# Kernel tuning notes

Measured on AMD Instinct MI355X. Metric: run time of the kernel, lower is better.

The kernel has to match this reference:

```python
import jax, jax.numpy as jnp
import numpy as np


def setup_inputs() -> dict:
    key = jax.random.key(0)
    k1, k2 = jax.random.split(key)
    q_embed = jax.random.normal(k1, (1000, 1024), dtype=jnp.float32)      # (V, D)
    conv_feat = jax.random.normal(k2, (64, 1024, 800), dtype=jnp.float32)  # (B, D, T)
    return {"q_embed": q_embed, "conv_feat": conv_feat}


def reference(q_embed, conv_feat):
    # sim_scores: (B, V, T) = q_embed (V, D) @ conv_feat (B, D, T), no scaling
    sim_scores = jnp.einsum('vd,bdt->bvt', q_embed, conv_feat)
    attention_weights = jax.nn.softmax(sim_scores, axis=2)  # over T
    # context: (B, V, D) = weights (B, V, T) @ conv_feat^T (B, T, D)
    context_vector = jnp.einsum('bvt,bdt->bvd', attention_weights, conv_feat)
    return (context_vector, attention_weights)
```

## Files before the change

kernel.cpp:

```cpp
#include <hip/hip_runtime.h>
#include <hip/hip_bf16.h>

typedef short bf16x8 __attribute__((ext_vector_type(8)));
typedef float f32x4 __attribute__((ext_vector_type(4)));

#define NV 1000
#define ND 1024
#define NT 800
#define NB 64

__device__ inline unsigned short f32_bf16(float f) {
    unsigned u = __builtin_bit_cast(unsigned, f);
    return (unsigned short)((u + 0x7FFFu + ((u >> 16) & 1u)) >> 16);
}
__device__ inline void split_bf16(float f, unsigned short& h, unsigned short& l) {
    unsigned u = __builtin_bit_cast(unsigned, f);
    unsigned hb = (u + 0x7FFFu + ((u >> 16) & 1u)) >> 16;
    h = (unsigned short)hb;
    float hf = __builtin_bit_cast(float, hb << 16);
    float lf = f - hf;
    unsigned ul = __builtin_bit_cast(unsigned, lf);
    l = (unsigned short)((ul + 0x7FFFu + ((ul >> 16) & 1u)) >> 16);
}

__device__ inline void gload16(const void* g, void* l) {
    __builtin_amdgcn_global_load_lds(
        (const __attribute__((address_space(1))) unsigned int*)g,
        (__attribute__((address_space(3))) unsigned int*)l, 16, 0, 0);
}

__global__ __launch_bounds__(256) void prep_q(const float* __restrict__ Q,
                                              unsigned short* __restrict__ Qh,
                                              unsigned short* __restrict__ Ql) {
    int idx = blockIdx.x * 256 + threadIdx.x;
    int row = idx >> 8;
    int c4 = (idx & 255) << 2;
    float4 f = make_float4(0.f, 0.f, 0.f, 0.f);
    if (row < NV) f = *(const float4*)(Q + (size_t)row * ND + c4);
    unsigned short h0,h1,h2,h3,l0,l1,l2,l3;
    split_bf16(f.x,h0,l0); split_bf16(f.y,h1,l1);
    split_bf16(f.z,h2,l2); split_bf16(f.w,h3,l3);
    *(ushort4*)(Qh + (size_t)row * ND + c4) = make_ushort4(h0,h1,h2,h3);
    *(ushort4*)(Ql + (size_t)row * ND + c4) = make_ushort4(l0,l1,l2,l3);
}

__global__ __launch_bounds__(256) void prep_c(const float* __restrict__ C,
                                              unsigned short* __restrict__ Cth,
                                              unsigned short* __restrict__ Ctl,
                                              unsigned short* __restrict__ Cbf,
                                              int writeCbf) {
    const int dt = blockIdx.x;
    const int tt = blockIdx.y;
    const int b  = blockIdx.z;
    const int tid = threadIdx.x;
    __shared__ float T[64][33];
    const float* Cb = C + (size_t)b * ND * NT;
    const int d0 = dt * 64, t0 = tt * 32;
#pragma unroll
    for (int r = 0; r < 2; ++r) {
        int idx = r * 256 + tid;
        int row = idx >> 3;
        int c4 = (idx & 7) << 2;
        float4 f = *(const float4*)(Cb + (size_t)(d0 + row) * NT + t0 + c4);
        T[row][c4 + 0] = f.x; T[row][c4 + 1] = f.y;
        T[row][c4 + 2] = f.z; T[row][c4 + 3] = f.w;
        if (writeCbf) {
            *(ushort4*)(Cbf + ((size_t)b * ND + d0 + row) * NT + t0 + c4) =
                make_ushort4(f32_bf16(f.x), f32_bf16(f.y), f32_bf16(f.z), f32_bf16(f.w));
        }
    }
    __syncthreads();
#pragma unroll
    for (int r = 0; r < 2; ++r) {
        int idx = r * 256 + tid;
        int trow = idx >> 4;
        int dc = (idx & 15) << 2;
        unsigned short h[4], l[4];
#pragma unroll
        for (int j = 0; j < 4; ++j) split_bf16(T[dc + j][trow], h[j], l[j]);
        size_t o = ((size_t)b * NT + t0 + trow) * ND + d0 + dc;
        *(ushort4*)(Cth + o) = make_ushort4(h[0],h[1],h[2],h[3]);
        *(ushort4*)(Ctl + o) = make_ushort4(l[0],l[1],l[2],l[3]);
    }
}

__global__ __launch_bounds__(512) void gemm1_kernel(const unsigned short* __restrict__ Qh,
                                                    const unsigned short* __restrict__ Ql,
                                                    const unsigned short* __restrict__ Cth,
                                                    const unsigned short* __restrict__ Ctl,
                                                    float* __restrict__ S) {
    const int h = blockIdx.x;
    const int L = (h & 7) * 160 + (h >> 3);
    const int bm = L & 3;
    const int rest = L >> 2;
    const int bn = rest % 5;
    const int b  = rest / 5;

    const int tid = threadIdx.x;
    const int lane = tid & 63;
    const int w = tid >> 6;
    const int wr = w >> 1, wc = w & 1;

    __shared__ unsigned short lds[2 * 26624];

    const int v0 = bm * 256, t0 = bn * 160;
    const unsigned short* Agh = Qh + (size_t)v0 * ND;
    const unsigned short* Agl = Ql + (size_t)v0 * ND;
    const unsigned short* Bgh = Cth + ((size_t)b * NT + t0) * ND;
    const unsigned short* Bgl = Ctl + ((size_t)b * NT + t0) * ND;

    f32x4 acc[4][5];
#pragma unroll
    for (int i = 0; i < 4; ++i)
#pragma unroll
        for (int j = 0; j < 5; ++j) acc[i][j] = (f32x4){0.f, 0.f, 0.f, 0.f};

    const int srow = lane >> 2;
    const int sslot = lane & 3;
    const int swz = (sslot ^ (srow & 3) ^ ((srow >> 2) & 3)) << 3;
    const int g = lane >> 4, rl = lane & 15;
    const int sx = (g ^ (rl & 3) ^ ((rl >> 2) & 3)) << 4;

    const unsigned short* srcB[7];
    int dstU[7];
#pragma unroll
    for (int j = 0; j < 7; ++j) {
        int R = w * 7 + j; if (R >= 52) R -= 52;
        const unsigned short* sp; int du;
        if (R < 16)      { sp = Agh + (size_t)(R * 16 + srow) * ND;          du = R * 512; }
        else if (R < 32) { sp = Agl + (size_t)((R - 16) * 16 + srow) * ND;   du = 8192 + (R - 16) * 512; }
        else if (R < 42) { sp = Bgh + (size_t)((R - 32) * 16 + srow) * ND;   du = 16384 + (R - 32) * 512; }
        else             { sp = Bgl + (size_t)((R - 42) * 16 + srow) * ND;   du = 21504 + (R - 42) * 512; }
        srcB[j] = sp + swz;
        dstU[j] = du;
    }

#define G1_STAGE(K0, BUF)                                                     \
    {                                                                         \
        unsigned short* Lb = lds + (BUF) * 26624;                             \
        _Pragma("unroll")                                                     \
        for (int j = 0; j < 7; ++j) gload16(srcB[j] + (K0), Lb + dstU[j]);    \
    }

#define G1_COMPUTE(BUF)                                                       \
    {                                                                         \
        const char* Lb = (const char*)(lds + (BUF) * 26624);                  \
        bf16x8 ah[4], al[4], bh[5], bl[5];                                    \
        _Pragma("unroll")                                                     \
        for (int mf = 0; mf < 4; ++mf) {                                      \
            int off = (wr * 64 + mf * 16 + rl) * 64 + sx;                     \
            ah[mf] = *(const bf16x8*)(Lb + off);                              \
            al[mf] = *(const bf16x8*)(Lb + 16384 + off);                      \
        }                                                                     \
        _Pragma("unroll")                                                     \
        for (int nf = 0; nf < 5; ++nf) {                                      \
            int off = (wc * 80 + nf * 16 + rl) * 64 + sx;                     \
            bh[nf] = *(const bf16x8*)(Lb + 32768 + off);                      \
            bl[nf] = *(const bf16x8*)(Lb + 43008 + off);                      \
        }                                                                     \
        _Pragma("unroll")                                                     \
        for (int mf = 0; mf < 4; ++mf)                                        \
            _Pragma("unroll")                                                 \
            for (int nf = 0; nf < 5; ++nf) {                                  \
                acc[mf][nf] = __builtin_amdgcn_mfma_f32_16x16x32_bf16(ah[mf], bh[nf], acc[mf][nf], 0, 0, 0); \
                acc[mf][nf] = __builtin_amdgcn_mfma_f32_16x16x32_bf16(ah[mf], bl[nf], acc[mf][nf], 0, 0, 0); \
                acc[mf][nf] = __builtin_amdgcn_mfma_f32_16x16x32_bf16(al[mf], bh[nf], acc[mf][nf], 0, 0, 0); \
            }                                                                 \
    }

    G1_STAGE(0, 0);
    int cur = 0;
#pragma unroll 1
    for (int t = 0; t < 31; ++t) {
        G1_STAGE((t + 1) * 32, cur ^ 1);
        asm volatile("s_waitcnt vmcnt(7)\n\ts_barrier" ::: "memory");
        G1_COMPUTE(cur);
        asm volatile("s_waitcnt lgkmcnt(0)\n\ts_barrier" ::: "memory");
        cur ^= 1;
    }
    asm volatile("s_waitcnt vmcnt(0)\n\ts_barrier" ::: "memory");
    G1_COMPUTE(cur);

    float* Sb = S + (size_t)b * NV * NT;
#pragma unroll
    for (int mf = 0; mf < 4; ++mf) {
#pragma unroll
        for (int nf = 0; nf < 5; ++nf) {
#pragma unroll
            for (int r = 0; r < 4; ++r) {
                int v = v0 + wr * 64 + mf * 16 + g * 4 + r;
                int t = t0 + wc * 80 + nf * 16 + rl;
                if (v < NV) Sb[(size_t)v * NT + t] = acc[mf][nf][r];
            }
        }
    }
#undef G1_STAGE
#undef G1_COMPUTE
}

__global__ __launch_bounds__(256) void softmax_kernel(float* __restrict__ S,
                                                      unsigned short* __restrict__ Wbf,
                                                      int writeWbf) {
    const int row = blockIdx.x * 4 + (threadIdx.x >> 6);
    const int lane = threadIdx.x & 63;
    float* p = S + (size_t)row * NT;
    unsigned short* pw = Wbf + (size_t)row * NT;
    float v[13];
    float m = -INFINITY;
#pragma unroll
    for (int i = 0; i < 13; ++i) {
        int t = i * 64 + lane;
        v[i] = (t < NT) ? p[t] : -INFINITY;
        m = fmaxf(m, v[i]);
    }
#pragma unroll
    for (int off = 32; off; off >>= 1) m = fmaxf(m, __shfl_xor(m, off));
    float s = 0.f;
#pragma unroll
    for (int i = 0; i < 13; ++i) {
        int t = i * 64 + lane;
        float e = (t < NT) ? __expf(v[i] - m) : 0.f;
        v[i] = e;
        s += e;
    }
#pragma unroll
    for (int off = 32; off; off >>= 1) s += __shfl_xor(s, off);
    const float inv = 1.0f / s;
#pragma unroll
    for (int i = 0; i < 13; ++i) {
        int t = i * 64 + lane;
        if (t < NT) {
            float wv = v[i] * inv;
            p[t] = wv;
            if (writeWbf) pw[t] = f32_bf16(wv);
        }
    }
}

__global__ __launch_bounds__(512) void gemm2_fast(const unsigned short* __restrict__ Wbf,
                                                  const unsigned short* __restrict__ Cbf,
                                                  float* __restrict__ O) {
    const int h = blockIdx.x;
    const int L = (h & 7) * 128 + (h >> 3);
    const int b  = L >> 4;
    const int bm = (L >> 2) & 3;
    const int bn = L & 3;
    const int tid = threadIdx.x;
    const int lane = tid & 63;
    const int w = tid >> 6;
    const int wr = w >> 2, wc = w & 3;

    __shared__ unsigned short lds[2 * 16384];

    const int v0 = bm * 256, d0 = bn * 256;
    const unsigned short* Ag = Wbf + (size_t)b * NV * NT;
    const unsigned short* Bg = Cbf + ((size_t)b * ND + d0) * NT;

    f32x4 acc[8][4];
#pragma unroll
    for (int i = 0; i < 8; ++i)
#pragma unroll
        for (int j = 0; j < 4; ++j) acc[i][j] = (f32x4){0.f, 0.f, 0.f, 0.f};

    const int srow = lane >> 2;
    const int sslot = lane & 3;
    const int swz = (sslot ^ (srow & 3) ^ ((srow >> 2) & 3)) << 3;
    const int g = lane >> 4, rl = lane & 15;
    const int sx = (g ^ (rl & 3) ^ ((rl >> 2) & 3)) << 4;

#define G2_STAGE(K0, BUF)                                                     \
    {                                                                         \
        unsigned short* Lb = lds + (BUF) * 16384;                             \
        _Pragma("unroll")                                                     \
        for (int i = w; i < 16; i += 8) {                                     \
            int row = i * 16 + srow;                                          \
            int vrow = v0 + row; if (vrow > NV - 1) vrow = NV - 1;            \
            gload16(Ag + (size_t)vrow * NT + swz + (K0), Lb + i * 512);       \
            gload16(Bg + (size_t)row * NT + swz + (K0), Lb + 8192 + i * 512); \
        }                                                                     \
    }

#define G2_COMPUTE(BUF)                                                       \
    {                                                                         \
        const char* Lb = (const char*)(lds + (BUF) * 16384);                  \
        bf16x8 a[8], bq[4];                                                   \
        _Pragma("unroll")                                                     \
        for (int mf = 0; mf < 8; ++mf) {                                      \
            int off = (wr * 128 + mf * 16 + rl) * 64 + sx;                    \
            a[mf] = *(const bf16x8*)(Lb + off);                               \
        }                                                                     \
        _Pragma("unroll")                                                     \
        for (int nf = 0; nf < 4; ++nf) {                                      \
            int off = (wc * 64 + nf * 16 + rl) * 64 + sx;                     \
            bq[nf] = *(const bf16x8*)(Lb + 16384 + off);                      \
        }                                                                     \
        _Pragma("unroll")                                                     \
        for (int mf = 0; mf < 8; ++mf)                                        \
            _Pragma("unroll")                                                 \
            for (int nf = 0; nf < 4; ++nf)                                    \
                acc[mf][nf] = __builtin_amdgcn_mfma_f32_16x16x32_bf16(a[mf], bq[nf], acc[mf][nf], 0, 0, 0); \
    }

    G2_STAGE(0, 0);
    int cur = 0;
#pragma unroll 1
    for (int t = 0; t < 24; ++t) {
        G2_STAGE((t + 1) * 32, cur ^ 1);
        asm volatile("s_waitcnt vmcnt(4)\n\ts_barrier" ::: "memory");
        G2_COMPUTE(cur);
        asm volatile("s_waitcnt lgkmcnt(0)\n\ts_barrier" ::: "memory");
        cur ^= 1;
    }
    asm volatile("s_waitcnt vmcnt(0)\n\ts_barrier" ::: "memory");
    G2_COMPUTE(cur);

    float* Ob = O + (size_t)b * NV * ND;
#pragma unroll
    for (int mf = 0; mf < 8; ++mf) {
#pragma unroll
        for (int nf = 0; nf < 4; ++nf) {
#pragma unroll
            for (int r = 0; r < 4; ++r) {
                int v = v0 + wr * 128 + mf * 16 + g * 4 + r;
                int d = d0 + wc * 64 + nf * 16 + rl;
                if (v < NV) Ob[(size_t)v * ND + d] = acc[mf][nf][r];
            }
        }
    }
#undef G2_STAGE
#undef G2_COMPUTE
}

__global__ __launch_bounds__(256) void gemm2_mid(const unsigned short* __restrict__ Wbf,
                                                 const float* __restrict__ C,
                                                 float* __restrict__ O) {
    const int h = blockIdx.x;
    const int L = (h & 7) * 512 + (h >> 3);
    const int bm = L & 7;
    const int bn = (L >> 3) & 7;
    const int b  = L >> 6;
    const int tid = threadIdx.x;
    const int lane = tid & 63;
    const int w = tid >> 6;
    const int wr = w >> 1, wc = w & 1;

    __shared__ unsigned short As[128 * 32];
    __shared__ unsigned short Bs[128][40];

    const int v0 = bm * 128, d0 = bn * 128;
    const unsigned short* Ag = Wbf + (size_t)b * NV * NT;
    const float* Cb = C + (size_t)b * ND * NT;

    f32x4 acc[4][4];
#pragma unroll
    for (int i = 0; i < 4; ++i)
#pragma unroll
        for (int j = 0; j < 4; ++j) acc[i][j] = (f32x4){0.f, 0.f, 0.f, 0.f};

    const int srow = lane >> 2;
    const int sslot = lane & 3;

    for (int k0 = 0; k0 < NT; k0 += 32) {
        for (int i = w; i < 8; i += 4) {
            int row = i * 16 + srow;
            int c = ((sslot ^ (row & 3)) << 3) + k0;
            int vrow = v0 + row; if (vrow > NV - 1) vrow = NV - 1;
            gload16(Ag + (size_t)vrow * NT + c, As + i * 512);
        }
#pragma unroll
        for (int r = 0; r < 4; ++r) {
            int idx = r * 256 + tid;
            int row = idx >> 3;
            int kq  = (idx & 7) << 2;
            const float4 f = *(const float4*)(Cb + (size_t)(d0 + row) * NT + k0 + kq);
            *(ushort4*)&Bs[row][kq] = make_ushort4(f32_bf16(f.x), f32_bf16(f.y), f32_bf16(f.z), f32_bf16(f.w));
        }
        __syncthreads();

        const int g = lane >> 4, rl = lane & 15;
        const int sx = (g ^ (rl & 3)) << 4;
        const int kk = g << 3;
        bf16x8 a[4], bfr[4];
#pragma unroll
        for (int mf = 0; mf < 4; ++mf) {
            int off = (wr * 64 + mf * 16 + rl) * 64 + sx;
            a[mf] = *(const bf16x8*)((const char*)As + off);
        }
#pragma unroll
        for (int nf = 0; nf < 4; ++nf) {
            int row = wc * 64 + nf * 16 + rl;
            bfr[nf] = *(const bf16x8*)&Bs[row][kk];
        }
#pragma unroll
        for (int mf = 0; mf < 4; ++mf)
#pragma unroll
            for (int nf = 0; nf < 4; ++nf)
                acc[mf][nf] = __builtin_amdgcn_mfma_f32_16x16x32_bf16(a[mf], bfr[nf], acc[mf][nf], 0, 0, 0);
        __syncthreads();
    }

    float* Ob = O + (size_t)b * NV * ND;
    const int g = lane >> 4, rl = lane & 15;
#pragma unroll
    for (int mf = 0; mf < 4; ++mf) {
#pragma unroll
        for (int nf = 0; nf < 4; ++nf) {
#pragma unroll
            for (int r = 0; r < 4; ++r) {
                int v = v0 + wr * 64 + mf * 16 + g * 4 + r;
                int d = d0 + wc * 64 + nf * 16 + rl;
                if (v < NV) Ob[(size_t)v * ND + d] = acc[mf][nf][r];
            }
        }
    }
}

__global__ __launch_bounds__(256) void gemm2_slow(const float* __restrict__ W,
                                                  const float* __restrict__ C,
                                                  float* __restrict__ O) {
    const int h = blockIdx.x;
    const int L = (h & 7) * 512 + (h >> 3);
    const int bm = L & 7;
    const int bn = (L >> 3) & 7;
    const int b  = L >> 6;
    const int tid = threadIdx.x;
    const int lane = tid & 63;
    const int wid = tid >> 6;
    const int wr = wid >> 1;
    const int wc = wid & 1;

    __shared__ unsigned short As[128][40];
    __shared__ unsigned short Bs[128][40];

    const float* Wb = W + (size_t)b * NV * NT;
    const float* Cb = C + (size_t)b * ND * NT;
    const int v0 = bm * 128;
    const int d0 = bn * 128;

    f32x4 acc[4][4];
#pragma unroll
    for (int i = 0; i < 4; ++i)
#pragma unroll
        for (int j = 0; j < 4; ++j) acc[i][j] = (f32x4){0.f, 0.f, 0.f, 0.f};

    for (int k0 = 0; k0 < NT; k0 += 32) {
#pragma unroll
        for (int r = 0; r < 4; ++r) {
            int idx = r * 256 + tid;
            int row = idx >> 3;
            int kq  = (idx & 7) << 2;
            int v = v0 + row; if (v > NV - 1) v = NV - 1;
            const float4 f = *(const float4*)(Wb + (size_t)v * NT + k0 + kq);
            *(ushort4*)&As[row][kq] = make_ushort4(f32_bf16(f.x), f32_bf16(f.y), f32_bf16(f.z), f32_bf16(f.w));
        }
#pragma unroll
        for (int r = 0; r < 4; ++r) {
            int idx = r * 256 + tid;
            int row = idx >> 3;
            int kq  = (idx & 7) << 2;
            const float4 f = *(const float4*)(Cb + (size_t)(d0 + row) * NT + k0 + kq);
            *(ushort4*)&Bs[row][kq] = make_ushort4(f32_bf16(f.x), f32_bf16(f.y), f32_bf16(f.z), f32_bf16(f.w));
        }
        __syncthreads();

        bf16x8 a[4], bfr[4];
        const int kk = (lane >> 4) << 3;
#pragma unroll
        for (int mf = 0; mf < 4; ++mf) {
            int row = wr * 64 + mf * 16 + (lane & 15);
            a[mf] = *(const bf16x8*)&As[row][kk];
        }
#pragma unroll
        for (int nf = 0; nf < 4; ++nf) {
            int row = wc * 64 + nf * 16 + (lane & 15);
            bfr[nf] = *(const bf16x8*)&Bs[row][kk];
        }
#pragma unroll
        for (int mf = 0; mf < 4; ++mf)
#pragma unroll
            for (int nf = 0; nf < 4; ++nf)
                acc[mf][nf] = __builtin_amdgcn_mfma_f32_16x16x32_bf16(a[mf], bfr[nf], acc[mf][nf], 0, 0, 0);
        __syncthreads();
    }

    float* Ob = O + (size_t)b * NV * ND;
#pragma unroll
    for (int mf = 0; mf < 4; ++mf) {
#pragma unroll
        for (int nf = 0; nf < 4; ++nf) {
#pragma unroll
            for (int r = 0; r < 4; ++r) {
                int v = v0 + wr * 64 + mf * 16 + (lane >> 4) * 4 + r;
                int d = d0 + wc * 64 + nf * 16 + (lane & 15);
                if (v < NV) Ob[(size_t)v * ND + d] = acc[mf][nf][r];
            }
        }
    }
}

extern "C" void kernel_launch(void* const* d_in, const int* in_sizes, int n_in,
                              void* d_out, int out_size, void* d_ws, size_t ws_size,
                              hipStream_t stream) {
    const float* Q = (const float*)d_in[0];
    const float* C = (const float*)d_in[1];
    float* ctx = (float*)d_out;
    float* wts = ctx + (size_t)NB * NV * ND;

    unsigned short* Cth = (unsigned short*)ctx;
    unsigned short* Ctl = Cth + (size_t)NB * NT * ND;
    unsigned short* Qh  = Ctl + (size_t)NB * NT * ND;
    unsigned short* Ql  = Qh + (size_t)1024 * ND;

    const size_t WbfBytes = (size_t)NB * NV * NT * 2;
    const size_t CbfBytes = (size_t)NB * ND * NT * 2;
    unsigned short* Wbf = (unsigned short*)d_ws;
    unsigned short* Cbf = (unsigned short*)((char*)d_ws + WbfBytes);
    const int wsFast = ws_size >= WbfBytes + CbfBytes;
    const int wsMid  = ws_size >= WbfBytes;

    prep_q<<<dim3(1024), 256, 0, stream>>>(Q, Qh, Ql);
    prep_c<<<dim3(16, 25, NB), 256, 0, stream>>>(C, Cth, Ctl, Cbf, wsFast);
    gemm1_kernel<<<dim3(1280), 512, 0, stream>>>(Qh, Ql, Cth, Ctl, wts);
    softmax_kernel<<<dim3(16000), 256, 0, stream>>>(wts, Wbf, wsMid);
    if (wsFast)      gemm2_fast<<<dim3(1024), 512, 0, stream>>>(Wbf, Cbf, ctx);
    else if (wsMid)  gemm2_mid<<<dim3(4096), 256, 0, stream>>>(Wbf, C, ctx);
    else             gemm2_slow<<<dim3(4096), 256, 0, stream>>>(wts, C, ctx);
}
```

Before: 658.1 us.

## Split GEMM inner loops into barrier-separated phases with MFMA priority; vectorize softmax

Both bf16 GEMM kernels now run their inner step as several phases. Each phase loads part of the LDS fragments, then issues MFMAs at raised s_setprio, with barriers and sched_barriers between phases. The goal is a ping-pong schedule in which one wave's LDS reads overlap with another wave's matrix math, and register pressure drops because fewer fragments are live at once. The cost is many more workgroup barriers per K step, which can serialize waves. Softmax is also switched to float4 loads and stores with packed bf16 writes, to cut memory instructions.

```diff
diff --git a/kernel.cpp b/kernel.cpp
--- a/kernel.cpp
+++ b/kernel.cpp
@@ -8,6 +8,9 @@
 #define ND 1024
 #define NT 800
 #define NB 64
+
+#define BARRIER asm volatile("s_barrier" ::: "memory")
+#define SB0 __builtin_amdgcn_sched_barrier(0)
 
 __device__ inline unsigned short f32_bf16(float f) {
     unsigned u = __builtin_bit_cast(unsigned, f);
@@ -135,6 +138,8 @@
         dstU[j] = du;
     }
 
+    bf16x8 ah[4], al[4], bh[5], bl[5];
+
 #define G1_STAGE(K0, BUF)                                                     \
     {                                                                         \
         unsigned short* Lb = lds + (BUF) * 26624;                             \
@@ -142,30 +147,45 @@
         for (int j = 0; j < 7; ++j) gload16(srcB[j] + (K0), Lb + dstU[j]);    \
     }
 
-#define G1_COMPUTE(BUF)                                                       \
+#define G1_PHASES(BUF)                                                        \
     {                                                                         \
         const char* Lb = (const char*)(lds + (BUF) * 26624);                  \
-        bf16x8 ah[4], al[4], bh[5], bl[5];                                    \
-        _Pragma("unroll")                                                     \
-        for (int mf = 0; mf < 4; ++mf) {                                      \
-            int off = (wr * 64 + mf * 16 + rl) * 64 + sx;                     \
-            ah[mf] = *(const bf16x8*)(Lb + off);                              \
-            al[mf] = *(const bf16x8*)(Lb + 16384 + off);                      \
-        }                                                                     \
-        _Pragma("unroll")                                                     \
-        for (int nf = 0; nf < 5; ++nf) {                                      \
-            int off = (wc * 80 + nf * 16 + rl) * 64 + sx;                     \
-            bh[nf] = *(const bf16x8*)(Lb + 32768 + off);                      \
-            bl[nf] = *(const bf16x8*)(Lb + 43008 + off);                      \
-        }                                                                     \
+        _Pragma("unroll")                                                     \
+        for (int mf = 0; mf < 4; ++mf)                                        \
+            ah[mf] = *(const bf16x8*)(Lb + (wr * 64 + mf * 16 + rl) * 64 + sx); \
+        _Pragma("unroll")                                                     \
+        for (int nf = 0; nf < 5; ++nf)                                        \
+            bh[nf] = *(const bf16x8*)(Lb + 32768 + (wc * 80 + nf * 16 + rl) * 64 + sx); \
+        BARRIER; SB0;                                                         \
+        __builtin_amdgcn_s_setprio(1);                                        \
         _Pragma("unroll")                                                     \
         for (int mf = 0; mf < 4; ++mf)                                        \
             _Pragma("unroll")                                                 \
-            for (int nf = 0; nf < 5; ++nf) {                                  \
+            for (int nf = 0; nf < 5; ++nf)                                    \
                 acc[mf][nf] = __builtin_amdgcn_mfma_f32_16x16x32_bf16(ah[mf], bh[nf], acc[mf][nf], 0, 0, 0); \
+        __builtin_amdgcn_s_setprio(0); SB0; BARRIER;                          \
+        _Pragma("unroll")                                                     \
+        for (int mf = 0; mf < 4; ++mf)                                        \
+            al[mf] = *(const bf16x8*)(Lb + 16384 + (wr * 64 + mf * 16 + rl) * 64 + sx); \
+        BARRIER; SB0;                                                         \
+        __builtin_amdgcn_s_setprio(1);                                        \
+        _Pragma("unroll")                                                     \
+        for (int mf = 0; mf < 4; ++mf)                                        \
+            _Pragma("unroll")                                                 \
+            for (int nf = 0; nf < 5; ++nf)                                    \
+                acc[mf][nf] = __builtin_amdgcn_mfma_f32_16x16x32_bf16(al[mf], bh[nf], acc[mf][nf], 0, 0, 0); \
+        __builtin_amdgcn_s_setprio(0); SB0; BARRIER;                          \
+        _Pragma("unroll")                                                     \
+        for (int nf = 0; nf < 5; ++nf)                                        \
+            bl[nf] = *(const bf16x8*)(Lb + 43008 + (wc * 80 + nf * 16 + rl) * 64 + sx); \
+        BARRIER; SB0;                                                         \
+        __builtin_amdgcn_s_setprio(1);                                        \
+        _Pragma("unroll")                                                     \
+        for (int mf = 0; mf < 4; ++mf)                                        \
+            _Pragma("unroll")                                                 \
+            for (int nf = 0; nf < 5; ++nf)                                    \
                 acc[mf][nf] = __builtin_amdgcn_mfma_f32_16x16x32_bf16(ah[mf], bl[nf], acc[mf][nf], 0, 0, 0); \
-                acc[mf][nf] = __builtin_amdgcn_mfma_f32_16x16x32_bf16(al[mf], bh[nf], acc[mf][nf], 0, 0, 0); \
-            }                                                                 \
+        __builtin_amdgcn_s_setprio(0); SB0; BARRIER;                          \
     }
 
     G1_STAGE(0, 0);
@@ -173,13 +193,14 @@
 #pragma unroll 1
     for (int t = 0; t < 31; ++t) {
         G1_STAGE((t + 1) * 32, cur ^ 1);
-        asm volatile("s_waitcnt vmcnt(7)\n\ts_barrier" ::: "memory");
-        G1_COMPUTE(cur);
-        asm volatile("s_waitcnt lgkmcnt(0)\n\ts_barrier" ::: "memory");
+        asm volatile("s_waitcnt vmcnt(7)" ::: "memory");
+        BARRIER;
+        G1_PHASES(cur);
         cur ^= 1;
     }
-    asm volatile("s_waitcnt vmcnt(0)\n\ts_barrier" ::: "memory");
-    G1_COMPUTE(cur);
+    asm volatile("s_waitcnt vmcnt(0)" ::: "memory");
+    BARRIER;
+    G1_PHASES(cur);
 
     float* Sb = S + (size_t)b * NV * NT;
 #pragma unroll
@@ -195,7 +216,7 @@
         }
     }
 #undef G1_STAGE
-#undef G1_COMPUTE
+#undef G1_PHASES
 }
 
 __global__ __launch_bounds__(256) void softmax_kernel(float* __restrict__ S,
@@ -203,36 +224,42 @@
                                                       int writeWbf) {
     const int row = blockIdx.x * 4 + (threadIdx.x >> 6);
     const int lane = threadIdx.x & 63;
-    float* p = S + (size_t)row * NT;
+    float4* p4 = (float4*)(S + (size_t)row * NT);
     unsigned short* pw = Wbf + (size_t)row * NT;
-    float v[13];
+    float4 v[4];
     float m = -INFINITY;
 #pragma unroll
-    for (int i = 0; i < 13; ++i) {
-        int t = i * 64 + lane;
-        v[i] = (t < NT) ? p[t] : -INFINITY;
-        m = fmaxf(m, v[i]);
+    for (int i = 0; i < 4; ++i) {
+        int idx = i * 64 + lane;
+        if (idx < 200) {
+            v[i] = p4[idx];
+            m = fmaxf(m, fmaxf(fmaxf(v[i].x, v[i].y), fmaxf(v[i].z, v[i].w)));
+        }
     }
 #pragma unroll
     for (int off = 32; off; off >>= 1) m = fmaxf(m, __shfl_xor(m, off));
     float s = 0.f;
 #pragma unroll
-    for (int i = 0; i < 13; ++i) {
-        int t = i * 64 + lane;
-        float e = (t < NT) ? __expf(v[i] - m) : 0.f;
-        v[i] = e;
-        s += e;
+    for (int i = 0; i < 4; ++i) {
+        int idx = i * 64 + lane;
+        if (idx < 200) {
+            v[i].x = __expf(v[i].x - m); v[i].y = __expf(v[i].y - m);
+            v[i].z = __expf(v[i].z - m); v[i].w = __expf(v[i].w - m);
+            s += (v[i].x + v[i].y) + (v[i].z + v[i].w);
+        }
     }
 #pragma unroll
     for (int off = 32; off; off >>= 1) s += __shfl_xor(s, off);
     const float inv = 1.0f / s;
 #pragma unroll
-    for (int i = 0; i < 13; ++i) {
-        int t = i * 64 + lane;
-        if (t < NT) {
-            float wv = v[i] * inv;
-            p[t] = wv;
-            if (writeWbf) pw[t] = f32_bf16(wv);
+    for (int i = 0; i < 4; ++i) {
+        int idx = i * 64 + lane;
+        if (idx < 200) {
+            float4 o = make_float4(v[i].x * inv, v[i].y * inv, v[i].z * inv, v[i].w * inv);
+            p4[idx] = o;
+            if (writeWbf)
+                *(ushort4*)(pw + idx * 4) =
+                    make_ushort4(f32_bf16(o.x), f32_bf16(o.y), f32_bf16(o.z), f32_bf16(o.w));
         }
     }
 }
@@ -268,6 +295,8 @@
     const int g = lane >> 4, rl = lane & 15;
     const int sx = (g ^ (rl & 3) ^ ((rl >> 2) & 3)) << 4;
 
+    bf16x8 a2[8], bq2[4];
+
 #define G2_STAGE(K0, BUF)                                                     \
     {                                                                         \
         unsigned short* Lb = lds + (BUF) * 16384;                             \
@@ -280,25 +309,34 @@
         }                                                                     \
     }
 
-#define G2_COMPUTE(BUF)                                                       \
+#define G2_PHASES(BUF)                                                        \
     {                                                                         \
         const char* Lb = (const char*)(lds + (BUF) * 16384);                  \
-        bf16x8 a[8], bq[4];                                                   \
-        _Pragma("unroll")                                                     \
-        for (int mf = 0; mf < 8; ++mf) {                                      \
-            int off = (wr * 128 + mf * 16 + rl) * 64 + sx;                    \
-            a[mf] = *(const bf16x8*)(Lb + off);                               \
-        }                                                                     \
-        _Pragma("unroll")                                                     \
-        for (int nf = 0; nf < 4; ++nf) {                                      \
-            int off = (wc * 64 + nf * 16 + rl) * 64 + sx;                     \
-            bq[nf] = *(const bf16x8*)(Lb + 16384 + off);                      \
-        }                                                                     \
-        _Pragma("unroll")                                                     \
-        for (int mf = 0; mf < 8; ++mf)                                        \
+        _Pragma("unroll")                                                     \
+        for (int mf = 0; mf < 4; ++mf)                                        \
+            a2[mf] = *(const bf16x8*)(Lb + (wr * 128 + mf * 16 + rl) * 64 + sx); \
+        _Pragma("unroll")                                                     \
+        for (int nf = 0; nf < 4; ++nf)                                        \
+            bq2[nf] = *(const bf16x8*)(Lb + 16384 + (wc * 64 + nf * 16 + rl) * 64 + sx); \
+        BARRIER; SB0;                                                         \
+        __builtin_amdgcn_s_setprio(1);                                        \
+        _Pragma("unroll")                                                     \
+        for (int mf = 0; mf < 4; ++mf)                                        \
             _Pragma("unroll")                                                 \
             for (int nf = 0; nf < 4; ++nf)                                    \
-                acc[mf][nf] = __builtin_amdgcn_mfma_f32_16x16x32_bf16(a[mf], bq[nf], acc[mf][nf], 0, 0, 0); \
+                acc[mf][nf] = __builtin_amdgcn_mfma_f32_16x16x32_bf16(a2[mf], bq2[nf], acc[mf][nf], 0, 0, 0); \
+        __builtin_amdgcn_s_setprio(0); SB0; BARRIER;                          \
+        _Pragma("unroll")                                                     \
+        for (int mf = 4; mf < 8; ++mf)                                        \
+            a2[mf] = *(const bf16x8*)(Lb + (wr * 128 + mf * 16 + rl) * 64 + sx); \
+        BARRIER; SB0;                                                         \
+        __builtin_amdgcn_s_setprio(1);                                        \
+        _Pragma("unroll")                                                     \
+        for (int mf = 4; mf < 8; ++mf)                                        \
+            _Pragma("unroll")                                                 \
+            for (int nf = 0; nf < 4; ++nf)                                    \
+                acc[mf][nf] = __builtin_amdgcn_mfma_f32_16x16x32_bf16(a2[mf], bq2[nf], acc[mf][nf], 0, 0, 0); \
+        __builtin_amdgcn_s_setprio(0); SB0; BARRIER;                          \
     }
 
     G2_STAGE(0, 0);
@@ -306,13 +344,14 @@
 #pragma unroll 1
     for (int t = 0; t < 24; ++t) {
         G2_STAGE((t + 1) * 32, cur ^ 1);
-        asm volatile("s_waitcnt vmcnt(4)\n\ts_barrier" ::: "memory");
-        G2_COMPUTE(cur);
-        asm volatile("s_waitcnt lgkmcnt(0)\n\ts_barrier" ::: "memory");
+        asm volatile("s_waitcnt vmcnt(4)" ::: "memory");
+        BARRIER;
+        G2_PHASES(cur);
         cur ^= 1;
     }
-    asm volatile("s_waitcnt vmcnt(0)\n\ts_barrier" ::: "memory");
-    G2_COMPUTE(cur);
+    asm volatile("s_waitcnt vmcnt(0)" ::: "memory");
+    BARRIER;
+    G2_PHASES(cur);
 
     float* Ob = O + (size_t)b * NV * ND;
 #pragma unroll
@@ -328,7 +367,7 @@
         }
     }
 #undef G2_STAGE
-#undef G2_COMPUTE
+#undef G2_PHASES
 }
 
 __global__ __launch_bounds__(256) void gemm2_mid(const unsigned short* __restrict__ Wbf,
```

Measured after the change: 705.4 us. 7.2% more time.
